# Optimization experiments

Hardware: AMD Instinct MI355X
Metric: run time of the kernel (lower is better)

## Reference

```python
import jax, jax.numpy as jnp
import numpy as np

B, N, K, H, NODE_IN, EDGE_IN, DEPTH = 4, 2000, 32, 128, 128, 128, 3
SCALE = 30.0
EPS = 1e-6


def layer_norm(x, g, b):
    mu = jnp.mean(x, axis=-1, keepdims=True)
    sigma = jnp.sqrt(jnp.var(x, axis=-1, ddof=1, keepdims=True) + EPS)
    return g * (x - mu) / (sigma + EPS) + b


def gather_nodes(nodes, idx):
    # nodes: [B,N,C], idx: [B,N,K] -> [B,N,K,C]
    b, n, k = idx.shape
    flat = idx.reshape(b, n * k)
    g = jnp.take_along_axis(nodes, flat[:, :, None], axis=1)
    return g.reshape(b, n, k, nodes.shape[-1])


def setup_inputs() -> dict:
    key = jax.random.key(0)
    ks = jax.random.split(key, 24)
    s = lambda fi, fo: 1.0 / np.sqrt(fi)
    inp = {
        'V': jax.random.normal(ks[0], (B, N, NODE_IN), jnp.float32),
        'E': jax.random.normal(ks[1], (B, N, K, EDGE_IN), jnp.float32),
        'hS': jax.random.normal(ks[2], (B, N, H), jnp.float32),
        'E_idx': jax.random.randint(ks[3], (B, N, K), 0, N, jnp.int64),
        'mask': jnp.ones((B, N), jnp.float32),
        'Wv_w': jax.random.normal(ks[4], (NODE_IN, H), jnp.float32) * s(NODE_IN, H),
        'Wv_b': jnp.zeros((H,), jnp.float32),
        'Wv_g': jnp.ones((H,), jnp.float32),
        'Wv_beta': jnp.zeros((H,), jnp.float32),
        'We_w': jax.random.normal(ks[5], (EDGE_IN, H), jnp.float32) * s(EDGE_IN, H),
        'We_b': jnp.zeros((H,), jnp.float32),
        'We_g': jnp.ones((H,), jnp.float32),
        'We_beta': jnp.zeros((H,), jnp.float32),
        'L_W1': jax.random.normal(ks[6], (DEPTH, 4 * H, H), jnp.float32) * s(4 * H, H),
        'L_b1': jnp.zeros((DEPTH, H), jnp.float32),
        'L_W2': jax.random.normal(ks[7], (DEPTH, H, H), jnp.float32) * s(H, H),
        'L_b2': jnp.zeros((DEPTH, H), jnp.float32),
        'L_W3': jax.random.normal(ks[8], (DEPTH, H, H), jnp.float32) * s(H, H),
        'L_b3': jnp.zeros((DEPTH, H), jnp.float32),
        'L_g': jnp.ones((DEPTH, H), jnp.float32),
        'L_beta': jnp.zeros((DEPTH, H), jnp.float32),
    }
    return inp


def reference(V, E, hS, E_idx, mask, Wv_w, Wv_b, Wv_g, Wv_beta,
              We_w, We_b, We_g, We_beta,
              L_W1, L_b1, L_W2, L_b2, L_W3, L_b3, L_g, L_beta):
    h_v = layer_norm(V @ Wv_w + Wv_b, Wv_g, Wv_beta)          # [B,N,H]
    h_e = layer_norm(E @ We_w + We_b, We_g, We_beta)          # [B,N,K,H]
    nei_s = gather_nodes(hS, E_idx)                            # [B,N,K,H]
    vmask = gather_nodes(mask[..., None], E_idx)[..., 0]       # [B,N,K]
    h = h_v
    for l in range(DEPTH):
        nei_v = gather_nodes(h, E_idx)                         # [B,N,K,H]
        h_exp = jnp.broadcast_to(h[:, :, None, :], nei_v.shape)
        h_ev = jnp.concatenate([h_exp, nei_v, nei_s, h_e], axis=-1)  # [B,N,K,4H]
        m = jax.nn.relu(h_ev @ L_W1[l] + L_b1[l])
        m = jax.nn.relu(m @ L_W2[l] + L_b2[l])
        m = m @ L_W3[l] + L_b3[l]
        m = vmask[..., None] * m
        dh = jnp.sum(m, axis=-2) / SCALE
        h = layer_norm(h + dh, L_g[l], L_beta[l])
        h = h * mask[..., None]
    return h
```

## Files before the change

### kernel.cpp

```cpp
#include <hip/hip_runtime.h>
#include <hip/hip_bf16.h>

#define BB 4
#define NN 2000
#define KK 32
#define HH 128
#define DEPTHL 3
constexpr int   SS   = 132;
constexpr float EPSF = 1e-6f;
constexpr float INV_SCALE = 1.0f / 30.0f;

typedef __attribute__((ext_vector_type(8))) short bf16x8;
typedef __attribute__((ext_vector_type(4))) short bf16x4;
typedef __attribute__((ext_vector_type(4))) float f32x4;

__device__ __forceinline__ float bf2f(unsigned short u) {
  union { unsigned int i; float f; } v; v.i = ((unsigned int)u) << 16; return v.f;
}
__device__ __forceinline__ unsigned short f2bf(float f) {
  union { float f; unsigned int i; } v; v.f = f;
  unsigned int x = v.i;
  return (unsigned short)((x + 0x7FFFu + ((x >> 16) & 1u)) >> 16);
}

__device__ __forceinline__ void gemm_acc(const float* __restrict__ lds,
                                         const float* __restrict__ Wp,
                                         int c0, int r0, float acc[8][2]) {
  for (int i = 0; i < HH; i += 4) {
    const float w00 = Wp[(i + 0) * HH + c0], w01 = Wp[(i + 0) * HH + c0 + 64];
    const float w10 = Wp[(i + 1) * HH + c0], w11 = Wp[(i + 1) * HH + c0 + 64];
    const float w20 = Wp[(i + 2) * HH + c0], w21 = Wp[(i + 2) * HH + c0 + 64];
    const float w30 = Wp[(i + 3) * HH + c0], w31 = Wp[(i + 3) * HH + c0 + 64];
#pragma unroll
    for (int r = 0; r < 8; r++) {
      const float4 a = *(const float4*)(lds + (r0 + r) * SS + i);
      acc[r][0] = fmaf(a.w, w30, fmaf(a.z, w20, fmaf(a.y, w10, fmaf(a.x, w00, acc[r][0]))));
      acc[r][1] = fmaf(a.w, w31, fmaf(a.z, w21, fmaf(a.y, w11, fmaf(a.x, w01, acc[r][1]))));
    }
  }
}

template <bool OUT_BF16>
__global__ __launch_bounds__(256) void proj_ln_kernel(
    const float* __restrict__ X, const float* __restrict__ W,
    const float* __restrict__ bias, const float* __restrict__ gam,
    const float* __restrict__ bet, void* __restrict__ outp) {
  __shared__ float seg[KK * SS];
  __shared__ float yb[KK * SS];
  const int t = threadIdx.x;
  const size_t row0 = (size_t)blockIdx.x * KK;

  {
    const int r = t >> 3, g8 = t & 7;
    const float* src = X + (row0 + r) * HH;
    float* dst = seg + r * SS;
#pragma unroll
    for (int ii = 0; ii < 4; ii++) {
      const int c = (g8 + 8 * ii) * 4;
      *(float4*)(dst + c) = *(const float4*)(src + c);
    }
  }
  __syncthreads();

  const int c0 = t & 63, rg = t >> 6, r0 = rg * 8;
  float acc[8][2];
  {
    const float b0 = bias[c0], b1v = bias[c0 + 64];
#pragma unroll
    for (int r = 0; r < 8; r++) { acc[r][0] = b0; acc[r][1] = b1v; }
  }
  gemm_acc(seg, W, c0, r0, acc);
#pragma unroll
  for (int r = 0; r < 8; r++) {
    yb[(r0 + r) * SS + c0]      = acc[r][0];
    yb[(r0 + r) * SS + c0 + 64] = acc[r][1];
  }
  __syncthreads();

  const int r = t >> 3, g8 = t & 7;
  float s = 0.f, q = 0.f;
#pragma unroll
  for (int ii = 0; ii < 4; ii++) {
    const int c = (g8 + 8 * ii) * 4;
    const float4 y = *(const float4*)(yb + r * SS + c);
    s += y.x + y.y + y.z + y.w;
    q += y.x * y.x + y.y * y.y + y.z * y.z + y.w * y.w;
  }
  s += __shfl_xor(s, 1); q += __shfl_xor(q, 1);
  s += __shfl_xor(s, 2); q += __shfl_xor(q, 2);
  s += __shfl_xor(s, 4); q += __shfl_xor(q, 4);
  const float mu  = s * (1.0f / HH);
  const float var = (q - (float)HH * mu * mu) * (1.0f / (HH - 1));
  const float inv = 1.0f / (sqrtf(var + EPSF) + EPSF);

#pragma unroll
  for (int ii = 0; ii < 4; ii++) {
    const int c = (g8 + 8 * ii) * 4;
    const float4 y = *(const float4*)(yb + r * SS + c);
    float o0 = gam[c + 0] * (y.x - mu) * inv + bet[c + 0];
    float o1 = gam[c + 1] * (y.y - mu) * inv + bet[c + 1];
    float o2 = gam[c + 2] * (y.z - mu) * inv + bet[c + 2];
    float o3 = gam[c + 3] * (y.w - mu) * inv + bet[c + 3];
    if (OUT_BF16) {
      ushort4 u;
      u.x = f2bf(o0); u.y = f2bf(o1); u.z = f2bf(o2); u.w = f2bf(o3);
      *(ushort4*)((unsigned short*)outp + (row0 + r) * HH + c) = u;
    } else {
      float4 o; o.x = o0; o.y = o1; o.z = o2; o.w = o3;
      *(float4*)((float*)outp + (row0 + r) * HH + c) = o;
    }
  }
}

__global__ __launch_bounds__(256) void wconv_kernel(
    const float* __restrict__ LW1, const float* __restrict__ LW2,
    const float* __restrict__ LW3, const float* __restrict__ Wew,
    unsigned short* __restrict__ WT) {
  const int gid = blockIdx.x * 256 + threadIdx.x;
  const int mat = gid >> 14;
  const int rem = gid & 16383;
  const int col = rem >> 7;
  const int k   = rem & 127;
  float v;
  if (mat == 9) {
    v = Wew[(size_t)k * HH + col];
  } else {
    const int l = mat / 3, wh = mat % 3;
    if (wh == 0)      v = LW1[(size_t)l * 4 * HH * HH + (size_t)(384 + k) * HH + col];
    else if (wh == 1) v = LW2[(size_t)l * HH * HH + (size_t)k * HH + col];
    else              v = LW3[(size_t)l * HH * HH + (size_t)k * HH + col];
  }
  WT[gid] = f2bf(v);
}

__global__ __launch_bounds__(256) void s1_kernel(
    const float* __restrict__ hS, const float* __restrict__ LW1,
    unsigned short* __restrict__ S1) {
  __shared__ float seg[KK * SS];
  const int t = threadIdx.x;
  const int l = blockIdx.x / 250;
  const size_t row0 = (size_t)(blockIdx.x % 250) * KK;
  {
    const int r = t >> 3, g8 = t & 7;
    const float* src = hS + (row0 + r) * HH;
    float* dst = seg + r * SS;
#pragma unroll
    for (int ii = 0; ii < 4; ii++) {
      const int c = (g8 + 8 * ii) * 4;
      *(float4*)(dst + c) = *(const float4*)(src + c);
    }
  }
  __syncthreads();
  const int c0 = t & 63, rg = t >> 6, r0 = rg * 8;
  float acc[8][2];
#pragma unroll
  for (int r = 0; r < 8; r++) { acc[r][0] = 0.f; acc[r][1] = 0.f; }
  gemm_acc(seg, LW1 + (size_t)l * 4 * HH * HH + 256 * HH, c0, r0, acc);
  unsigned short* out = S1 + (size_t)l * BB * NN * HH;
#pragma unroll
  for (int r = 0; r < 8; r++) {
    const size_t gr = (row0 + r0 + r) * HH;
    out[gr + c0]      = f2bf(acc[r][0]);
    out[gr + c0 + 64] = f2bf(acc[r][1]);
  }
}

__global__ __launch_bounds__(256) void node_pre_kernel(
    const float* __restrict__ h_in, const float* __restrict__ W1,
    const float* __restrict__ b1, const unsigned short* __restrict__ S1l,
    float* __restrict__ C1, unsigned short* __restrict__ G1) {
  __shared__ float seg[KK * SS];
  const int t = threadIdx.x;
  const size_t row0 = (size_t)blockIdx.x * KK;
  {
    const int r = t >> 3, g8 = t & 7;
    const float* src = h_in + (row0 + r) * HH;
    float* dst = seg + r * SS;
#pragma unroll
    for (int ii = 0; ii < 4; ii++) {
      const int c = (g8 + 8 * ii) * 4;
      *(float4*)(dst + c) = *(const float4*)(src + c);
    }
  }
  __syncthreads();
  const int c0 = t & 63, rg = t >> 6, r0 = rg * 8;
  float accC[8][2], accG[8][2];
  {
    const float b0 = b1[c0], b1v = b1[c0 + 64];
#pragma unroll
    for (int r = 0; r < 8; r++) {
      accC[r][0] = b0; accC[r][1] = b1v;
      accG[r][0] = 0.f; accG[r][1] = 0.f;
    }
  }
  gemm_acc(seg, W1, c0, r0, accC);
  gemm_acc(seg, W1 + 128 * HH, c0, r0, accG);
#pragma unroll
  for (int r = 0; r < 8; r++) {
    const size_t gr = (row0 + r0 + r) * HH;
    C1[gr + c0]      = accC[r][0];
    C1[gr + c0 + 64] = accC[r][1];
    G1[gr + c0]      = f2bf(accG[r][0] + bf2f(S1l[gr + c0]));
    G1[gr + c0 + 64] = f2bf(accG[r][1] + bf2f(S1l[gr + c0 + 64]));
  }
}

__device__ __forceinline__ bf16x8 ldsA(const unsigned short* T, int rf, int ks, int lr, int lg) {
  const int row = rf * 16 + lr;
  const int boff = (row * 256 + ks * 64 + lg * 16) ^ ((row & 7) << 4);
  return *(const bf16x8*)((const char*)T + boff);
}
__device__ __forceinline__ bf16x8 ldgB(const unsigned short* __restrict__ WT, int col, int ks, int lg) {
  return *(const bf16x8*)(WT + col * 128 + ks * 32 + lg * 8);
}

__global__ __launch_bounds__(256) void proj_ln_e_mfma(
    const float* __restrict__ E, const unsigned short* __restrict__ WeT,
    const float* __restrict__ bias, const float* __restrict__ gam,
    const float* __restrict__ bet, unsigned short* __restrict__ he) {
  __shared__ unsigned short T0[KK * HH];
  __shared__ float yb[KK * SS];
  __shared__ float biasS[HH];
  const int t = threadIdx.x;
  const size_t row0 = (size_t)blockIdx.x * KK;

  {
    const int row = t >> 3, cb = (t & 7) * 16;
    const float* src = E + (row0 + row) * HH + cb;
    const float4 f0 = *(const float4*)(src);
    const float4 f1 = *(const float4*)(src + 4);
    const float4 f2 = *(const float4*)(src + 8);
    const float4 f3 = *(const float4*)(src + 12);
    bf16x8 u0, u1;
    u0[0] = (short)f2bf(f0.x); u0[1] = (short)f2bf(f0.y); u0[2] = (short)f2bf(f0.z); u0[3] = (short)f2bf(f0.w);
    u0[4] = (short)f2bf(f1.x); u0[5] = (short)f2bf(f1.y); u0[6] = (short)f2bf(f1.z); u0[7] = (short)f2bf(f1.w);
    u1[0] = (short)f2bf(f2.x); u1[1] = (short)f2bf(f2.y); u1[2] = (short)f2bf(f2.z); u1[3] = (short)f2bf(f2.w);
    u1[4] = (short)f2bf(f3.x); u1[5] = (short)f2bf(f3.y); u1[6] = (short)f2bf(f3.z); u1[7] = (short)f2bf(f3.w);
    const int base = row * 256 + cb * 2;
    const int sw = (row & 7) << 4;
    *(bf16x8*)((char*)T0 + (base ^ sw)) = u0;
    *(bf16x8*)((char*)T0 + ((base + 16) ^ sw)) = u1;
  }
  if (t < HH) biasS[t] = bias[t];
  __syncthreads();

  const int lane = t & 63, wid = t >> 6, lr = lane & 15, lg = lane >> 4;
  const int wbase = wid * 32;
  f32x4 a00 = (f32x4){0.f,0.f,0.f,0.f}, a01 = a00, a10 = a00, a11 = a00;
#pragma unroll
  for (int ks = 0; ks < 4; ks++) {
    const bf16x8 fw0 = ldgB(WeT, wbase + lr, ks, lg);
    const bf16x8 fw1 = ldgB(WeT, wbase + 16 + lr, ks, lg);
    const bf16x8 ft0 = ldsA(T0, 0, ks, lr, lg);
    const bf16x8 ft1 = ldsA(T0, 1, ks, lr, lg);
    a00 = __builtin_amdgcn_mfma_f32_16x16x32_bf16(fw0, ft0, a00, 0, 0, 0);
    a01 = __builtin_amdgcn_mfma_f32_16x16x32_bf16(fw0, ft1, a01, 0, 0, 0);
    a10 = __builtin_amdgcn_mfma_f32_16x16x32_bf16(fw1, ft0, a10, 0, 0, 0);
    a11 = __builtin_amdgcn_mfma_f32_16x16x32_bf16(fw1, ft1, a11, 0, 0, 0);
  }
#pragma unroll
  for (int a = 0; a < 2; a++) {
    const int col0 = wbase + a * 16 + lg * 4;
    const float4 bv = *(const float4*)(biasS + col0);
#pragma unroll
    for (int b = 0; b < 2; b++) {
      const int edge = b * 16 + lr;
      const f32x4 ac = a == 0 ? (b == 0 ? a00 : a01) : (b == 0 ? a10 : a11);
      float4 y; y.x = ac[0] + bv.x; y.y = ac[1] + bv.y; y.z = ac[2] + bv.z; y.w = ac[3] + bv.w;
      *(float4*)(yb + edge * SS + col0) = y;
    }
  }
  __syncthreads();

  const int r = t >> 3, g8 = t & 7;
  float s = 0.f, q = 0.f;
#pragma unroll
  for (int ii = 0; ii < 4; ii++) {
    const int c = (g8 + 8 * ii) * 4;
    const float4 y = *(const float4*)(yb + r * SS + c);
    s += y.x + y.y + y.z + y.w;
    q += y.x * y.x + y.y * y.y + y.z * y.z + y.w * y.w;
  }
  s += __shfl_xor(s, 1); q += __shfl_xor(q, 1);
  s += __shfl_xor(s, 2); q += __shfl_xor(q, 2);
  s += __shfl_xor(s, 4); q += __shfl_xor(q, 4);
  const float mu  = s * (1.0f / HH);
  const float var = (q - (float)HH * mu * mu) * (1.0f / (HH - 1));
  const float inv = 1.0f / (sqrtf(var + EPSF) + EPSF);
#pragma unroll
  for (int ii = 0; ii < 4; ii++) {
    const int c = (g8 + 8 * ii) * 4;
    const float4 y = *(const float4*)(yb + r * SS + c);
    ushort4 u;
    u.x = f2bf(gam[c + 0] * (y.x - mu) * inv + bet[c + 0]);
    u.y = f2bf(gam[c + 1] * (y.y - mu) * inv + bet[c + 1]);
    u.z = f2bf(gam[c + 2] * (y.z - mu) * inv + bet[c + 2]);
    u.w = f2bf(gam[c + 3] * (y.w - mu) * inv + bet[c + 3]);
    *(ushort4*)(he + (row0 + r) * HH + c) = u;
  }
}

__global__ __launch_bounds__(512, 6) void edge_kernel(
    const float* __restrict__ h_in, const unsigned short* __restrict__ he,
    const int* __restrict__ E_idx, const float* __restrict__ mask,
    const float* __restrict__ C1, const unsigned short* __restrict__ G1,
    const unsigned short* __restrict__ WT1e, const unsigned short* __restrict__ WT2,
    const unsigned short* __restrict__ WT3,
    const float* __restrict__ b2, const float* __restrict__ b3,
    const float* __restrict__ gam, const float* __restrict__ bet,
    float* __restrict__ h_out) {
  __shared__ unsigned short T0[2][KK * HH];
  __shared__ unsigned short T1[2][KK * HH];
  __shared__ unsigned short G1s[2][KK * HH];
  __shared__ float C1s[2][HH], dhs[2][HH];
  __shared__ float b2s[HH], b3s[HH];
  __shared__ float svm[2][KK];
  __shared__ float redS[2][4], redQ[2][4];

  const int t = threadIdx.x;
  const int nh = t >> 8, tt = t & 255;
  const int node = blockIdx.x * 2 + nh;
  const int bbase = (node / NN) * NN;

  {
    const int row = tt >> 3, cb = (tt & 7) * 16;
    const unsigned short* hrow = he + ((size_t)node * KK + row) * HH + cb;
    const bf16x8 e0 = *(const bf16x8*)hrow;
    const bf16x8 e1 = *(const bf16x8*)(hrow + 8);
    const int base = row * 256 + cb * 2;
    const int sw = (row & 7) << 4;
    *(bf16x8*)((char*)T0[nh] + (base ^ sw)) = e0;
    *(bf16x8*)((char*)T0[nh] + ((base + 16) ^ sw)) = e1;
    const int nb = E_idx[(size_t)node * KK + row];
    const unsigned short* gsrc = G1 + (size_t)(bbase + nb) * HH + cb;
    const bf16x8 g0 = *(const bf16x8*)gsrc;
    const bf16x8 g1 = *(const bf16x8*)(gsrc + 8);
    *(bf16x8*)((char*)G1s[nh] + (base ^ sw)) = g0;
    *(bf16x8*)((char*)G1s[nh] + ((base + 16) ^ sw)) = g1;
  }
  if (tt < HH) C1s[nh][tt] = C1[(size_t)node * HH + tt];
  if (t < HH) b2s[t] = b2[t];
  else if (t < 2 * HH) b3s[t - HH] = b3[t - HH];
  if (tt < KK) svm[nh][tt] = mask[bbase + E_idx[(size_t)node * KK + tt]];
  __syncthreads();

  const int lane = tt & 63, wid = tt >> 6, lr = lane & 15, lg = lane >> 4;
  const int wbase = wid * 32;
  f32x4 a00, a01, a10, a11;

#define ZERO_ACC() do { a00 = (f32x4){0.f,0.f,0.f,0.f}; a01 = a00; a10 = a00; a11 = a00; } while (0)
#define DO_GEMM_T(TILE, WTm) do {                                          \
    _Pragma("unroll")                                                      \
    for (int ks = 0; ks < 4; ks++) {                                       \
      const bf16x8 fw0 = ldgB(WTm, wbase + lr, ks, lg);                    \
      const bf16x8 fw1 = ldgB(WTm, wbase + 16 + lr, ks, lg);               \
      const bf16x8 ft0 = ldsA(TILE, 0, ks, lr, lg);                        \
      const bf16x8 ft1 = ldsA(TILE, 1, ks, lr, lg);                        \
      a00 = __builtin_amdgcn_mfma_f32_16x16x32_bf16(fw0, ft0, a00, 0, 0, 0); \
      a01 = __builtin_amdgcn_mfma_f32_16x16x32_bf16(fw0, ft1, a01, 0, 0, 0); \
      a10 = __builtin_amdgcn_mfma_f32_16x16x32_bf16(fw1, ft0, a10, 0, 0, 0); \
      a11 = __builtin_amdgcn_mfma_f32_16x16x32_bf16(fw1, ft1, a11, 0, 0, 0); \
    } } while (0)

  ZERO_ACC();
  DO_GEMM_T(T0[nh], WT1e);
#pragma unroll
  for (int a = 0; a < 2; a++) {
    const int col0 = wbase + a * 16 + lg * 4;
    const float4 c1v = *(const float4*)(&C1s[nh][col0]);
#pragma unroll
    for (int b = 0; b < 2; b++) {
      const int edge = b * 16 + lr;
      const int boff = (edge * 256 + col0 * 2) ^ ((edge & 7) << 4);
      const bf16x4 g = *(const bf16x4*)((const char*)G1s[nh] + boff);
      const f32x4 ac = a == 0 ? (b == 0 ? a00 : a01) : (b == 0 ? a10 : a11);
      const float x0 = fmaxf(ac[0] + c1v.x + bf2f((unsigned short)g[0]), 0.f);
      const float x1 = fmaxf(ac[1] + c1v.y + bf2f((unsigned short)g[1]), 0.f);
      const float x2 = fmaxf(ac[2] + c1v.z + bf2f((unsigned short)g[2]), 0.f);
      const float x3 = fmaxf(ac[3] + c1v.w + bf2f((unsigned short)g[3]), 0.f);
      uint2 pv;
      pv.x = (unsigned)f2bf(x0) | ((unsigned)f2bf(x1) << 16);
      pv.y = (unsigned)f2bf(x2) | ((unsigned)f2bf(x3) << 16);
      *(uint2*)((char*)T1[nh] + boff) = pv;
    }
  }
  __syncthreads();

  ZERO_ACC();
  DO_GEMM_T(T1[nh], WT2);
#pragma unroll
  for (int a = 0; a < 2; a++) {
    const int col0 = wbase + a * 16 + lg * 4;
    const float4 bv = *(const float4*)(b2s + col0);
#pragma unroll
    for (int b = 0; b < 2; b++) {
      const int edge = b * 16 + lr;
      const int boff = (edge * 256 + col0 * 2) ^ ((edge & 7) << 4);
      const f32x4 ac = a == 0 ? (b == 0 ? a00 : a01) : (b == 0 ? a10 : a11);
      const float x0 = fmaxf(ac[0] + bv.x, 0.f);
      const float x1 = fmaxf(ac[1] + bv.y, 0.f);
      const float x2 = fmaxf(ac[2] + bv.z, 0.f);
      const float x3 = fmaxf(ac[3] + bv.w, 0.f);
      uint2 pv;
      pv.x = (unsigned)f2bf(x0) | ((unsigned)f2bf(x1) << 16);
      pv.y = (unsigned)f2bf(x2) | ((unsigned)f2bf(x3) << 16);
      *(uint2*)((char*)T0[nh] + boff) = pv;
    }
  }
  __syncthreads();

  ZERO_ACC();
  {
    const int col0 = wbase + lr, col1 = wbase + 16 + lr;
#pragma unroll
    for (int ks = 0; ks < 4; ks++) {
      const bf16x8 fa0 = ldsA(T0[nh], 0, ks, lr, lg);
      const bf16x8 fa1 = ldsA(T0[nh], 1, ks, lr, lg);
      const bf16x8 fb0 = ldgB(WT3, col0, ks, lg);
      const bf16x8 fb1 = ldgB(WT3, col1, ks, lg);
      a00 = __builtin_amdgcn_mfma_f32_16x16x32_bf16(fa0, fb0, a00, 0, 0, 0);
      a01 = __builtin_amdgcn_mfma_f32_16x16x32_bf16(fa0, fb1, a01, 0, 0, 0);
      a10 = __builtin_amdgcn_mfma_f32_16x16x32_bf16(fa1, fb0, a10, 0, 0, 0);
      a11 = __builtin_amdgcn_mfma_f32_16x16x32_bf16(fa1, fb1, a11, 0, 0, 0);
    }
    const float cb0 = b3s[col0], cb1 = b3s[col1];
    float s0 = 0.f, s1 = 0.f;
#pragma unroll
    for (int rf = 0; rf < 2; rf++) {
      const f32x4 v0 = rf ? a10 : a00;
      const f32x4 v1 = rf ? a11 : a01;
#pragma unroll
      for (int r = 0; r < 4; r++) {
        const int edge = rf * 16 + lg * 4 + r;
        const float vm = svm[nh][edge];
        s0 += vm * (v0[r] + cb0);
        s1 += vm * (v1[r] + cb1);
      }
    }
    s0 += __shfl_xor(s0, 16); s0 += __shfl_xor(s0, 32);
    s1 += __shfl_xor(s1, 16); s1 += __shfl_xor(s1, 32);
    if (lg == 0) { dhs[nh][col0] = s0; dhs[nh][col1] = s1; }
  }
  __syncthreads();

  float v = 0.f;
  if (tt < HH) v = h_in[(size_t)node * HH + tt] + dhs[nh][tt] * INV_SCALE;
  float s = (tt < HH) ? v : 0.f;
  float q = (tt < HH) ? v * v : 0.f;
#pragma unroll
  for (int off = 32; off >= 1; off >>= 1) { s += __shfl_xor(s, off); q += __shfl_xor(q, off); }
  if ((tt & 63) == 0) { redS[nh][tt >> 6] = s; redQ[nh][tt >> 6] = q; }
  __syncthreads();
  if (tt < HH) {
    const float S = redS[nh][0] + redS[nh][1] + redS[nh][2] + redS[nh][3];
    const float Q = redQ[nh][0] + redQ[nh][1] + redQ[nh][2] + redQ[nh][3];
    const float mu  = S * (1.0f / HH);
    const float var = (Q - (float)HH * mu * mu) * (1.0f / (HH - 1));
    const float inv = 1.0f / (sqrtf(var + EPSF) + EPSF);
    h_out[(size_t)node * HH + tt] = (gam[tt] * (v - mu) * inv + bet[tt]) * mask[node];
  }
#undef ZERO_ACC
#undef DO_GEMM_T
}

extern "C" void kernel_launch(void* const* d_in, const int* in_sizes, int n_in,
                              void* d_out, int out_size, void* d_ws, size_t ws_size,
                              hipStream_t stream) {
  const float* V     = (const float*)d_in[0];
  const float* E     = (const float*)d_in[1];
  const float* hS    = (const float*)d_in[2];
  const int*   Eidx  = (const int*)d_in[3];
  const float* mask  = (const float*)d_in[4];
  const float* Wv_w  = (const float*)d_in[5];
  const float* Wv_b  = (const float*)d_in[6];
  const float* Wv_g  = (const float*)d_in[7];
  const float* Wv_be = (const float*)d_in[8];
  const float* We_w  = (const float*)d_in[9];
  const float* We_b  = (const float*)d_in[10];
  const float* We_g  = (const float*)d_in[11];
  const float* We_be = (const float*)d_in[12];
  const float* LW1   = (const float*)d_in[13];
  const float* Lb1   = (const float*)d_in[14];
  const float* LW2   = (const float*)d_in[15];
  const float* Lb2   = (const float*)d_in[16];
  const float* LW3   = (const float*)d_in[17];
  const float* Lb3   = (const float*)d_in[18];
  const float* Lg    = (const float*)d_in[19];
  const float* Lbe   = (const float*)d_in[20];

  char* w = (char*)d_ws;
  unsigned short* he  = (unsigned short*)(w);
  unsigned short* S1  = (unsigned short*)(w + 65536000);
  float* C1           = (float*)(w + 71680000);
  unsigned short* G1  = (unsigned short*)(w + 75776000);
  unsigned short* WT  = (unsigned short*)(w + 77824000);
  float* h0           = (float*)(w + 78151680);
  float* h1           = (float*)(w + 82247680);

  wconv_kernel<<<dim3(640), dim3(256), 0, stream>>>(LW1, LW2, LW3, We_w, WT);
  s1_kernel<<<dim3(750), dim3(256), 0, stream>>>(hS, LW1, S1);
  proj_ln_kernel<false><<<dim3((BB * NN) / KK), dim3(256), 0, stream>>>(
      V, Wv_w, Wv_b, Wv_g, Wv_be, (void*)h0);
  proj_ln_e_mfma<<<dim3((BB * NN * KK) / KK), dim3(256), 0, stream>>>(
      E, WT + (size_t)9 * HH * HH, We_b, We_g, We_be, he);

  const float* hin = h0;
  float* bufs[2] = { h1, h0 };
  for (int l = 0; l < DEPTHL; l++) {
    node_pre_kernel<<<dim3(250), dim3(256), 0, stream>>>(
        hin, LW1 + (size_t)l * 4 * HH * HH, Lb1 + (size_t)l * HH,
        S1 + (size_t)l * BB * NN * HH, C1, G1);
    float* out = (l == DEPTHL - 1) ? (float*)d_out : bufs[l & 1];
    edge_kernel<<<dim3(BB * NN / 2), dim3(512), 0, stream>>>(
        hin, he, Eidx, mask, C1, G1,
        WT + (size_t)(l * 3 + 0) * HH * HH,
        WT + (size_t)(l * 3 + 1) * HH * HH,
        WT + (size_t)(l * 3 + 2) * HH * HH,
        Lb2 + (size_t)l * HH, Lb3 + (size_t)l * HH,
        Lg + (size_t)l * HH, Lbe + (size_t)l * HH, out);
    hin = out;
  }
}
```

Before: 699.5 us.

## Move node projections to bf16 MFMA, drop S1 kernel, reuse edge LDS buffer

Replaces the scalar fp32 GEMMs in the V projection and per-layer node precompute with bf16 MFMA kernels, using pre-converted transposed weights from an extended weight-conversion kernel. The hS contribution is now computed inside the per-layer node kernel, so the separate S1 kernel and its buffer go away. In the edge kernel the T1 LDS tile is dropped and the G1s buffer is reused for the first hidden activation, and the occupancy hint is raised from 6 to 8. This lowers fp32 ALU work and LDS footprint. In exchange the node-side products lose precision to bf16, and the hS GEMM is recomputed every layer.

```diff
diff --git a/kernel.cpp b/kernel.cpp
--- a/kernel.cpp
+++ b/kernel.cpp
@@ -23,57 +23,101 @@
   return (unsigned short)((x + 0x7FFFu + ((x >> 16) & 1u)) >> 16);
 }
 
-__device__ __forceinline__ void gemm_acc(const float* __restrict__ lds,
-                                         const float* __restrict__ Wp,
-                                         int c0, int r0, float acc[8][2]) {
-  for (int i = 0; i < HH; i += 4) {
-    const float w00 = Wp[(i + 0) * HH + c0], w01 = Wp[(i + 0) * HH + c0 + 64];
-    const float w10 = Wp[(i + 1) * HH + c0], w11 = Wp[(i + 1) * HH + c0 + 64];
-    const float w20 = Wp[(i + 2) * HH + c0], w21 = Wp[(i + 2) * HH + c0 + 64];
-    const float w30 = Wp[(i + 3) * HH + c0], w31 = Wp[(i + 3) * HH + c0 + 64];
-#pragma unroll
-    for (int r = 0; r < 8; r++) {
-      const float4 a = *(const float4*)(lds + (r0 + r) * SS + i);
-      acc[r][0] = fmaf(a.w, w30, fmaf(a.z, w20, fmaf(a.y, w10, fmaf(a.x, w00, acc[r][0]))));
-      acc[r][1] = fmaf(a.w, w31, fmaf(a.z, w21, fmaf(a.y, w11, fmaf(a.x, w01, acc[r][1]))));
-    }
-  }
+__global__ __launch_bounds__(256) void wconv_kernel(
+    const float* __restrict__ LW1, const float* __restrict__ LW2,
+    const float* __restrict__ LW3, const float* __restrict__ Wew,
+    const float* __restrict__ Wvw, unsigned short* __restrict__ WT) {
+  const int gid = blockIdx.x * 256 + threadIdx.x;
+  const int mat = gid >> 14;
+  const int rem = gid & 16383;
+  const int col = rem >> 7;
+  const int k   = rem & 127;
+  float v;
+  if (mat < 9) {
+    const int l = mat / 3, wh = mat % 3;
+    if (wh == 0)      v = LW1[(size_t)l * 4 * HH * HH + (size_t)(384 + k) * HH + col];
+    else if (wh == 1) v = LW2[(size_t)l * HH * HH + (size_t)k * HH + col];
+    else              v = LW3[(size_t)l * HH * HH + (size_t)k * HH + col];
+  } else if (mat == 9) {
+    v = Wew[(size_t)k * HH + col];
+  } else if (mat == 10) {
+    v = Wvw[(size_t)k * HH + col];
+  } else {
+    const int m = mat - 11;
+    const int grp = m / 3, l = m % 3;
+    v = LW1[(size_t)l * 4 * HH * HH + (size_t)(grp * 128 + k) * HH + col];
+  }
+  WT[gid] = f2bf(v);
+}
+
+__device__ __forceinline__ bf16x8 ldsA(const unsigned short* T, int rf, int ks, int lr, int lg) {
+  const int row = rf * 16 + lr;
+  const int boff = (row * 256 + ks * 64 + lg * 16) ^ ((row & 7) << 4);
+  return *(const bf16x8*)((const char*)T + boff);
+}
+__device__ __forceinline__ bf16x8 ldgB(const unsigned short* __restrict__ WT, int col, int ks, int lg) {
+  return *(const bf16x8*)(WT + col * 128 + ks * 32 + lg * 8);
+}
+
+__device__ __forceinline__ void stage_f32_tile(const float* __restrict__ src0,
+                                               unsigned short* __restrict__ T, int t) {
+  const int row = t >> 3, cb = (t & 7) * 16;
+  const float* src = src0 + row * HH + cb;
+  const float4 f0 = *(const float4*)(src);
+  const float4 f1 = *(const float4*)(src + 4);
+  const float4 f2 = *(const float4*)(src + 8);
+  const float4 f3 = *(const float4*)(src + 12);
+  bf16x8 u0, u1;
+  u0[0] = (short)f2bf(f0.x); u0[1] = (short)f2bf(f0.y); u0[2] = (short)f2bf(f0.z); u0[3] = (short)f2bf(f0.w);
+  u0[4] = (short)f2bf(f1.x); u0[5] = (short)f2bf(f1.y); u0[6] = (short)f2bf(f1.z); u0[7] = (short)f2bf(f1.w);
+  u1[0] = (short)f2bf(f2.x); u1[1] = (short)f2bf(f2.y); u1[2] = (short)f2bf(f2.z); u1[3] = (short)f2bf(f2.w);
+  u1[4] = (short)f2bf(f3.x); u1[5] = (short)f2bf(f3.y); u1[6] = (short)f2bf(f3.z); u1[7] = (short)f2bf(f3.w);
+  const int base = row * 256 + cb * 2;
+  const int sw = (row & 7) << 4;
+  *(bf16x8*)((char*)T + (base ^ sw)) = u0;
+  *(bf16x8*)((char*)T + ((base + 16) ^ sw)) = u1;
 }
 
 template <bool OUT_BF16>
-__global__ __launch_bounds__(256) void proj_ln_kernel(
-    const float* __restrict__ X, const float* __restrict__ W,
+__global__ __launch_bounds__(256) void proj_ln_x_mfma(
+    const float* __restrict__ X, const unsigned short* __restrict__ WxT,
     const float* __restrict__ bias, const float* __restrict__ gam,
     const float* __restrict__ bet, void* __restrict__ outp) {
-  __shared__ float seg[KK * SS];
+  __shared__ unsigned short T0[KK * HH];
   __shared__ float yb[KK * SS];
+  __shared__ float biasS[HH];
   const int t = threadIdx.x;
   const size_t row0 = (size_t)blockIdx.x * KK;
 
-  {
-    const int r = t >> 3, g8 = t & 7;
-    const float* src = X + (row0 + r) * HH;
-    float* dst = seg + r * SS;
-#pragma unroll
-    for (int ii = 0; ii < 4; ii++) {
-      const int c = (g8 + 8 * ii) * 4;
-      *(float4*)(dst + c) = *(const float4*)(src + c);
-    }
-  }
-  __syncthreads();
-
-  const int c0 = t & 63, rg = t >> 6, r0 = rg * 8;
-  float acc[8][2];
-  {
-    const float b0 = bias[c0], b1v = bias[c0 + 64];
-#pragma unroll
-    for (int r = 0; r < 8; r++) { acc[r][0] = b0; acc[r][1] = b1v; }
-  }
-  gemm_acc(seg, W, c0, r0, acc);
-#pragma unroll
-  for (int r = 0; r < 8; r++) {
-    yb[(r0 + r) * SS + c0]      = acc[r][0];
-    yb[(r0 + r) * SS + c0 + 64] = acc[r][1];
+  stage_f32_tile(X + row0 * HH, T0, t);
+  if (t < HH) biasS[t] = bias[t];
+  __syncthreads();
+
+  const int lane = t & 63, wid = t >> 6, lr = lane & 15, lg = lane >> 4;
+  const int wbase = wid * 32;
+  f32x4 a00 = (f32x4){0.f,0.f,0.f,0.f}, a01 = a00, a10 = a00, a11 = a00;
+#pragma unroll
+  for (int ks = 0; ks < 4; ks++) {
+    const bf16x8 fw0 = ldgB(WxT, wbase + lr, ks, lg);
+    const bf16x8 fw1 = ldgB(WxT, wbase + 16 + lr, ks, lg);
+    const bf16x8 ft0 = ldsA(T0, 0, ks, lr, lg);
+    const bf16x8 ft1 = ldsA(T0, 1, ks, lr, lg);
+    a00 = __builtin_amdgcn_mfma_f32_16x16x32_bf16(fw0, ft0, a00, 0, 0, 0);
+    a01 = __builtin_amdgcn_mfma_f32_16x16x32_bf16(fw0, ft1, a01, 0, 0, 0);
+    a10 = __builtin_amdgcn_mfma_f32_16x16x32_bf16(fw1, ft0, a10, 0, 0, 0);
+    a11 = __builtin_amdgcn_mfma_f32_16x16x32_bf16(fw1, ft1, a11, 0, 0, 0);
+  }
+#pragma unroll
+  for (int a = 0; a < 2; a++) {
+    const int col0 = wbase + a * 16 + lg * 4;
+    const float4 bv = *(const float4*)(biasS + col0);
+#pragma unroll
+    for (int b = 0; b < 2; b++) {
+      const int row = b * 16 + lr;
+      const f32x4 ac = a == 0 ? (b == 0 ? a00 : a01) : (b == 0 ? a10 : a11);
+      float4 y; y.x = ac[0] + bv.x; y.y = ac[1] + bv.y; y.z = ac[2] + bv.z; y.w = ac[3] + bv.w;
+      *(float4*)(yb + row * SS + col0) = y;
+    }
   }
   __syncthreads();
 
@@ -92,15 +136,14 @@
   const float mu  = s * (1.0f / HH);
   const float var = (q - (float)HH * mu * mu) * (1.0f / (HH - 1));
   const float inv = 1.0f / (sqrtf(var + EPSF) + EPSF);
-
 #pragma unroll
   for (int ii = 0; ii < 4; ii++) {
     const int c = (g8 + 8 * ii) * 4;
     const float4 y = *(const float4*)(yb + r * SS + c);
-    float o0 = gam[c + 0] * (y.x - mu) * inv + bet[c + 0];
-    float o1 = gam[c + 1] * (y.y - mu) * inv + bet[c + 1];
-    float o2 = gam[c + 2] * (y.z - mu) * inv + bet[c + 2];
-    float o3 = gam[c + 3] * (y.w - mu) * inv + bet[c + 3];
+    const float o0 = gam[c + 0] * (y.x - mu) * inv + bet[c + 0];
+    const float o1 = gam[c + 1] * (y.y - mu) * inv + bet[c + 1];
+    const float o2 = gam[c + 2] * (y.z - mu) * inv + bet[c + 2];
+    const float o3 = gam[c + 3] * (y.w - mu) * inv + bet[c + 3];
     if (OUT_BF16) {
       ushort4 u;
       u.x = f2bf(o0); u.y = f2bf(o1); u.z = f2bf(o2); u.w = f2bf(o3);
@@ -112,147 +155,33 @@
   }
 }
 
-__global__ __launch_bounds__(256) void wconv_kernel(
-    const float* __restrict__ LW1, const float* __restrict__ LW2,
-    const float* __restrict__ LW3, const float* __restrict__ Wew,
-    unsigned short* __restrict__ WT) {
-  const int gid = blockIdx.x * 256 + threadIdx.x;
-  const int mat = gid >> 14;
-  const int rem = gid & 16383;
-  const int col = rem >> 7;
-  const int k   = rem & 127;
-  float v;
-  if (mat == 9) {
-    v = Wew[(size_t)k * HH + col];
-  } else {
-    const int l = mat / 3, wh = mat % 3;
-    if (wh == 0)      v = LW1[(size_t)l * 4 * HH * HH + (size_t)(384 + k) * HH + col];
-    else if (wh == 1) v = LW2[(size_t)l * HH * HH + (size_t)k * HH + col];
-    else              v = LW3[(size_t)l * HH * HH + (size_t)k * HH + col];
-  }
-  WT[gid] = f2bf(v);
-}
-
-__global__ __launch_bounds__(256) void s1_kernel(
-    const float* __restrict__ hS, const float* __restrict__ LW1,
-    unsigned short* __restrict__ S1) {
-  __shared__ float seg[KK * SS];
-  const int t = threadIdx.x;
-  const int l = blockIdx.x / 250;
-  const size_t row0 = (size_t)(blockIdx.x % 250) * KK;
-  {
-    const int r = t >> 3, g8 = t & 7;
-    const float* src = hS + (row0 + r) * HH;
-    float* dst = seg + r * SS;
-#pragma unroll
-    for (int ii = 0; ii < 4; ii++) {
-      const int c = (g8 + 8 * ii) * 4;
-      *(float4*)(dst + c) = *(const float4*)(src + c);
-    }
-  }
-  __syncthreads();
-  const int c0 = t & 63, rg = t >> 6, r0 = rg * 8;
-  float acc[8][2];
-#pragma unroll
-  for (int r = 0; r < 8; r++) { acc[r][0] = 0.f; acc[r][1] = 0.f; }
-  gemm_acc(seg, LW1 + (size_t)l * 4 * HH * HH + 256 * HH, c0, r0, acc);
-  unsigned short* out = S1 + (size_t)l * BB * NN * HH;
-#pragma unroll
-  for (int r = 0; r < 8; r++) {
-    const size_t gr = (row0 + r0 + r) * HH;
-    out[gr + c0]      = f2bf(acc[r][0]);
-    out[gr + c0 + 64] = f2bf(acc[r][1]);
-  }
-}
-
-__global__ __launch_bounds__(256) void node_pre_kernel(
-    const float* __restrict__ h_in, const float* __restrict__ W1,
-    const float* __restrict__ b1, const unsigned short* __restrict__ S1l,
+__global__ __launch_bounds__(256) void node_pre_mfma(
+    const float* __restrict__ h_in, const float* __restrict__ hS,
+    const unsigned short* __restrict__ W1cT, const unsigned short* __restrict__ W1vT,
+    const unsigned short* __restrict__ W1sT, const float* __restrict__ b1,
     float* __restrict__ C1, unsigned short* __restrict__ G1) {
-  __shared__ float seg[KK * SS];
+  __shared__ unsigned short Th[KK * HH];
+  __shared__ unsigned short Ts[KK * HH];
+  __shared__ float b1s[HH];
   const int t = threadIdx.x;
   const size_t row0 = (size_t)blockIdx.x * KK;
-  {
-    const int r = t >> 3, g8 = t & 7;
-    const float* src = h_in + (row0 + r) * HH;
-    float* dst = seg + r * SS;
-#pragma unroll
-    for (int ii = 0; ii < 4; ii++) {
-      const int c = (g8 + 8 * ii) * 4;
-      *(float4*)(dst + c) = *(const float4*)(src + c);
-    }
-  }
-  __syncthreads();
-  const int c0 = t & 63, rg = t >> 6, r0 = rg * 8;
-  float accC[8][2], accG[8][2];
-  {
-    const float b0 = b1[c0], b1v = b1[c0 + 64];
-#pragma unroll
-    for (int r = 0; r < 8; r++) {
-      accC[r][0] = b0; accC[r][1] = b1v;
-      accG[r][0] = 0.f; accG[r][1] = 0.f;
-    }
-  }
-  gemm_acc(seg, W1, c0, r0, accC);
-  gemm_acc(seg, W1 + 128 * HH, c0, r0, accG);
-#pragma unroll
-  for (int r = 0; r < 8; r++) {
-    const size_t gr = (row0 + r0 + r) * HH;
-    C1[gr + c0]      = accC[r][0];
-    C1[gr + c0 + 64] = accC[r][1];
-    G1[gr + c0]      = f2bf(accG[r][0] + bf2f(S1l[gr + c0]));
-    G1[gr + c0 + 64] = f2bf(accG[r][1] + bf2f(S1l[gr + c0 + 64]));
-  }
-}
-
-__device__ __forceinline__ bf16x8 ldsA(const unsigned short* T, int rf, int ks, int lr, int lg) {
-  const int row = rf * 16 + lr;
-  const int boff = (row * 256 + ks * 64 + lg * 16) ^ ((row & 7) << 4);
-  return *(const bf16x8*)((const char*)T + boff);
-}
-__device__ __forceinline__ bf16x8 ldgB(const unsigned short* __restrict__ WT, int col, int ks, int lg) {
-  return *(const bf16x8*)(WT + col * 128 + ks * 32 + lg * 8);
-}
-
-__global__ __launch_bounds__(256) void proj_ln_e_mfma(
-    const float* __restrict__ E, const unsigned short* __restrict__ WeT,
-    const float* __restrict__ bias, const float* __restrict__ gam,
-    const float* __restrict__ bet, unsigned short* __restrict__ he) {
-  __shared__ unsigned short T0[KK * HH];
-  __shared__ float yb[KK * SS];
-  __shared__ float biasS[HH];
-  const int t = threadIdx.x;
-  const size_t row0 = (size_t)blockIdx.x * KK;
-
-  {
-    const int row = t >> 3, cb = (t & 7) * 16;
-    const float* src = E + (row0 + row) * HH + cb;
-    const float4 f0 = *(const float4*)(src);
-    const float4 f1 = *(const float4*)(src + 4);
-    const float4 f2 = *(const float4*)(src + 8);
-    const float4 f3 = *(const float4*)(src + 12);
-    bf16x8 u0, u1;
-    u0[0] = (short)f2bf(f0.x); u0[1] = (short)f2bf(f0.y); u0[2] = (short)f2bf(f0.z); u0[3] = (short)f2bf(f0.w);
-    u0[4] = (short)f2bf(f1.x); u0[5] = (short)f2bf(f1.y); u0[6] = (short)f2bf(f1.z); u0[7] = (short)f2bf(f1.w);
-    u1[0] = (short)f2bf(f2.x); u1[1] = (short)f2bf(f2.y); u1[2] = (short)f2bf(f2.z); u1[3] = (short)f2bf(f2.w);
-    u1[4] = (short)f2bf(f3.x); u1[5] = (short)f2bf(f3.y); u1[6] = (short)f2bf(f3.z); u1[7] = (short)f2bf(f3.w);
-    const int base = row * 256 + cb * 2;
-    const int sw = (row & 7) << 4;
-    *(bf16x8*)((char*)T0 + (base ^ sw)) = u0;
-    *(bf16x8*)((char*)T0 + ((base + 16) ^ sw)) = u1;
-  }
-  if (t < HH) biasS[t] = bias[t];
+
+  stage_f32_tile(h_in + row0 * HH, Th, t);
+  stage_f32_tile(hS + row0 * HH, Ts, t);
+  if (t < HH) b1s[t] = b1[t];
   __syncthreads();
 
   const int lane = t & 63, wid = t >> 6, lr = lane & 15, lg = lane >> 4;
   const int wbase = wid * 32;
-  f32x4 a00 = (f32x4){0.f,0.f,0.f,0.f}, a01 = a00, a10 = a00, a11 = a00;
+  f32x4 a00, a01, a10, a11;
+
+  a00 = (f32x4){0.f,0.f,0.f,0.f}; a01 = a00; a10 = a00; a11 = a00;
 #pragma unroll
   for (int ks = 0; ks < 4; ks++) {
-    const bf16x8 fw0 = ldgB(WeT, wbase + lr, ks, lg);
-    const bf16x8 fw1 = ldgB(WeT, wbase + 16 + lr, ks, lg);
-    const bf16x8 ft0 = ldsA(T0, 0, ks, lr, lg);
-    const bf16x8 ft1 = ldsA(T0, 1, ks, lr, lg);
+    const bf16x8 fw0 = ldgB(W1cT, wbase + lr, ks, lg);
+    const bf16x8 fw1 = ldgB(W1cT, wbase + 16 + lr, ks, lg);
+    const bf16x8 ft0 = ldsA(Th, 0, ks, lr, lg);
+    const bf16x8 ft1 = ldsA(Th, 1, ks, lr, lg);
     a00 = __builtin_amdgcn_mfma_f32_16x16x32_bf16(fw0, ft0, a00, 0, 0, 0);
     a01 = __builtin_amdgcn_mfma_f32_16x16x32_bf16(fw0, ft1, a01, 0, 0, 0);
     a10 = __builtin_amdgcn_mfma_f32_16x16x32_bf16(fw1, ft0, a10, 0, 0, 0);
@@ -261,46 +190,55 @@
 #pragma unroll
   for (int a = 0; a < 2; a++) {
     const int col0 = wbase + a * 16 + lg * 4;
-    const float4 bv = *(const float4*)(biasS + col0);
+    const float4 bv = *(const float4*)(b1s + col0);
 #pragma unroll
     for (int b = 0; b < 2; b++) {
-      const int edge = b * 16 + lr;
+      const int row = b * 16 + lr;
       const f32x4 ac = a == 0 ? (b == 0 ? a00 : a01) : (b == 0 ? a10 : a11);
       float4 y; y.x = ac[0] + bv.x; y.y = ac[1] + bv.y; y.z = ac[2] + bv.z; y.w = ac[3] + bv.w;
-      *(float4*)(yb + edge * SS + col0) = y;
-    }
-  }
-  __syncthreads();
-
-  const int r = t >> 3, g8 = t & 7;
-  float s = 0.f, q = 0.f;
-#pragma unroll
-  for (int ii = 0; ii < 4; ii++) {
-    const int c = (g8 + 8 * ii) * 4;
-    const float4 y = *(const float4*)(yb + r * SS + c);
-    s += y.x + y.y + y.z + y.w;
-    q += y.x * y.x + y.y * y.y + y.z * y.z + y.w * y.w;
-  }
-  s += __shfl_xor(s, 1); q += __shfl_xor(q, 1);
-  s += __shfl_xor(s, 2); q += __shfl_xor(q, 2);
-  s += __shfl_xor(s, 4); q += __shfl_xor(q, 4);
-  const float mu  = s * (1.0f / HH);
-  const float var = (q - (float)HH * mu * mu) * (1.0f / (HH - 1));
-  const float inv = 1.0f / (sqrtf(var + EPSF) + EPSF);
-#pragma unroll
-  for (int ii = 0; ii < 4; ii++) {
-    const int c = (g8 + 8 * ii) * 4;
-    const float4 y = *(const float4*)(yb + r * SS + c);
-    ushort4 u;
-    u.x = f2bf(gam[c + 0] * (y.x - mu) * inv + bet[c + 0]);
-    u.y = f2bf(gam[c + 1] * (y.y - mu) * inv + bet[c + 1]);
-    u.z = f2bf(gam[c + 2] * (y.z - mu) * inv + bet[c + 2]);
-    u.w = f2bf(gam[c + 3] * (y.w - mu) * inv + bet[c + 3]);
-    *(ushort4*)(he + (row0 + r) * HH + c) = u;
-  }
-}
-
-__global__ __launch_bounds__(512, 6) void edge_kernel(
+      *(float4*)(C1 + (row0 + row) * HH + col0) = y;
+    }
+  }
+
+  a00 = (f32x4){0.f,0.f,0.f,0.f}; a01 = a00; a10 = a00; a11 = a00;
+#pragma unroll
+  for (int ks = 0; ks < 4; ks++) {
+    const bf16x8 fw0 = ldgB(W1vT, wbase + lr, ks, lg);
+    const bf16x8 fw1 = ldgB(W1vT, wbase + 16 + lr, ks, lg);
+    const bf16x8 ft0 = ldsA(Th, 0, ks, lr, lg);
+    const bf16x8 ft1 = ldsA(Th, 1, ks, lr, lg);
+    a00 = __builtin_amdgcn_mfma_f32_16x16x32_bf16(fw0, ft0, a00, 0, 0, 0);
+    a01 = __builtin_amdgcn_mfma_f32_16x16x32_bf16(fw0, ft1, a01, 0, 0, 0);
+    a10 = __builtin_amdgcn_mfma_f32_16x16x32_bf16(fw1, ft0, a10, 0, 0, 0);
+    a11 = __builtin_amdgcn_mfma_f32_16x16x32_bf16(fw1, ft1, a11, 0, 0, 0);
+  }
+#pragma unroll
+  for (int ks = 0; ks < 4; ks++) {
+    const bf16x8 fw0 = ldgB(W1sT, wbase + lr, ks, lg);
+    const bf16x8 fw1 = ldgB(W1sT, wbase + 16 + lr, ks, lg);
+    const bf16x8 ft0 = ldsA(Ts, 0, ks, lr, lg);
+    const bf16x8 ft1 = ldsA(Ts, 1, ks, lr, lg);
+    a00 = __builtin_amdgcn_mfma_f32_16x16x32_bf16(fw0, ft0, a00, 0, 0, 0);
+    a01 = __builtin_amdgcn_mfma_f32_16x16x32_bf16(fw0, ft1, a01, 0, 0, 0);
+    a10 = __builtin_amdgcn_mfma_f32_16x16x32_bf16(fw1, ft0, a10, 0, 0, 0);
+    a11 = __builtin_amdgcn_mfma_f32_16x16x32_bf16(fw1, ft1, a11, 0, 0, 0);
+  }
+#pragma unroll
+  for (int a = 0; a < 2; a++) {
+    const int col0 = wbase + a * 16 + lg * 4;
+#pragma unroll
+    for (int b = 0; b < 2; b++) {
+      const int row = b * 16 + lr;
+      const f32x4 ac = a == 0 ? (b == 0 ? a00 : a01) : (b == 0 ? a10 : a11);
+      uint2 pv;
+      pv.x = (unsigned)f2bf(ac[0]) | ((unsigned)f2bf(ac[1]) << 16);
+      pv.y = (unsigned)f2bf(ac[2]) | ((unsigned)f2bf(ac[3]) << 16);
+      *(uint2*)(G1 + (row0 + row) * HH + col0) = pv;
+    }
+  }
+}
+
+__global__ __launch_bounds__(512, 8) void edge_kernel(
     const float* __restrict__ h_in, const unsigned short* __restrict__ he,
     const int* __restrict__ E_idx, const float* __restrict__ mask,
     const float* __restrict__ C1, const unsigned short* __restrict__ G1,
@@ -310,7 +248,6 @@
     const float* __restrict__ gam, const float* __restrict__ bet,
     float* __restrict__ h_out) {
   __shared__ unsigned short T0[2][KK * HH];
-  __shared__ unsigned short T1[2][KK * HH];
   __shared__ unsigned short G1s[2][KK * HH];
   __shared__ float C1s[2][HH], dhs[2][HH];
   __shared__ float b2s[HH], b3s[HH];
@@ -381,13 +318,13 @@
       uint2 pv;
       pv.x = (unsigned)f2bf(x0) | ((unsigned)f2bf(x1) << 16);
       pv.y = (unsigned)f2bf(x2) | ((unsigned)f2bf(x3) << 16);
-      *(uint2*)((char*)T1[nh] + boff) = pv;
+      *(uint2*)((char*)G1s[nh] + boff) = pv;
     }
   }
   __syncthreads();
 
   ZERO_ACC();
-  DO_GEMM_T(T1[nh], WT2);
+  DO_GEMM_T(G1s[nh], WT2);
 #pragma unroll
   for (int a = 0; a < 2; a++) {
     const int col0 = wbase + a * 16 + lg * 4;
@@ -490,26 +427,27 @@
 
   char* w = (char*)d_ws;
   unsigned short* he  = (unsigned short*)(w);
-  unsigned short* S1  = (unsigned short*)(w + 65536000);
-  float* C1           = (float*)(w + 71680000);
-  unsigned short* G1  = (unsigned short*)(w + 75776000);
-  unsigned short* WT  = (unsigned short*)(w + 77824000);
-  float* h0           = (float*)(w + 78151680);
-  float* h1           = (float*)(w + 82247680);
-
-  wconv_kernel<<<dim3(640), dim3(256), 0, stream>>>(LW1, LW2, LW3, We_w, WT);
-  s1_kernel<<<dim3(750), dim3(256), 0, stream>>>(hS, LW1, S1);
-  proj_ln_kernel<false><<<dim3((BB * NN) / KK), dim3(256), 0, stream>>>(
-      V, Wv_w, Wv_b, Wv_g, Wv_be, (void*)h0);
-  proj_ln_e_mfma<<<dim3((BB * NN * KK) / KK), dim3(256), 0, stream>>>(
-      E, WT + (size_t)9 * HH * HH, We_b, We_g, We_be, he);
+  float* C1           = (float*)(w + 65536000);
+  unsigned short* G1  = (unsigned short*)(w + 69632000);
+  unsigned short* WT  = (unsigned short*)(w + 71680000);
+  float* h0           = (float*)(w + 72335360);
+  float* h1           = (float*)(w + 76431360);
+
+  wconv_kernel<<<dim3(1280), dim3(256), 0, stream>>>(LW1, LW2, LW3, We_w, Wv_w, WT);
+  proj_ln_x_mfma<false><<<dim3((BB * NN) / KK), dim3(256), 0, stream>>>(
+      V, WT + (size_t)10 * HH * HH, Wv_b, Wv_g, Wv_be, (void*)h0);
+  proj_ln_x_mfma<true><<<dim3((BB * NN * KK) / KK), dim3(256), 0, stream>>>(
+      E, WT + (size_t)9 * HH * HH, We_b, We_g, We_be, (void*)he);
 
   const float* hin = h0;
   float* bufs[2] = { h1, h0 };
   for (int l = 0; l < DEPTHL; l++) {
-    node_pre_kernel<<<dim3(250), dim3(256), 0, stream>>>(
-        hin, LW1 + (size_t)l * 4 * HH * HH, Lb1 + (size_t)l * HH,
-        S1 + (size_t)l * BB * NN * HH, C1, G1);
+    node_pre_mfma<<<dim3(250), dim3(256), 0, stream>>>(
+        hin, hS,
+        WT + (size_t)(11 + 0 * 3 + l) * HH * HH,
+        WT + (size_t)(11 + 1 * 3 + l) * HH * HH,
+        WT + (size_t)(11 + 2 * 3 + l) * HH * HH,
+        Lb1 + (size_t)l * HH, C1, G1);
     float* out = (l == DEPTHL - 1) ? (float*)d_out : bufs[l & 1];
     edge_kernel<<<dim3(BB * NN / 2), dim3(512), 0, stream>>>(
         hin, he, Eidx, mask, C1, G1,
```

Result: faster. 608.8 us (-13.0%).
